# Kernel optimization log

Measured on AMD Instinct MI355X. Metric: run time of the kernel, lower is better.

The kernel has to match this reference:

```python
import jax, jax.numpy as jnp
import numpy as np
from jax import lax

B, S, D = 4, 2048, 512          # batch, doc seq len, input_size
Y = 8922                          # num labels (ICD codes)
V, E = 50000, 100                 # vocab, word embed dim
T, K = 32, 9                      # code-title tokens, conv filter size
PAD = K // 2


def setup_inputs() -> dict:
    key = jax.random.key(0)
    ks = jax.random.split(key, 8)
    x = jax.random.normal(ks[0], (B, S, D), dtype=jnp.float32)
    target = jax.random.randint(ks[1], (B, Y), 0, 2).astype(jnp.float32)
    c2title = jax.random.randint(ks[2], (Y, T), 0, V)
    embed_W = jax.random.normal(ks[3], (V, E), dtype=jnp.float32) * 0.1
    conv_w = jax.random.normal(ks[4], (D, E, K), dtype=jnp.float32) * 0.05  # [out, in, k]
    conv_b = jax.random.normal(ks[5], (D,), dtype=jnp.float32) * 0.05
    final_w = jax.random.normal(ks[6], (Y, D), dtype=jnp.float32) * 0.05
    final_b = jax.random.normal(ks[7], (Y,), dtype=jnp.float32) * 0.05
    return {"x": x, "target": target, "c2title": c2title, "embed_W": embed_W,
            "conv_w": conv_w, "conv_b": conv_b, "final_w": final_w, "final_b": final_b}


def reference(x, target, c2title, embed_W, conv_w, conv_b, final_w, final_b):
    # Code-title encoder: embed -> Conv1d (same padding) -> max-pool over time -> tanh
    ct = embed_W[c2title]                      # [Y, T, E]
    ct = jnp.transpose(ct, (0, 2, 1))          # [Y, E, T]  (NCH)
    U = lax.conv_general_dilated(ct, conv_w, window_strides=(1,),
                                 padding=[(PAD, PAD)],
                                 dimension_numbers=("NCH", "OIH", "NCH"))
    U = U + conv_b[None, :, None]              # [Y, D, T]
    U = jnp.tanh(jnp.max(U, axis=-1))          # [Y, D]  (MaxPool1d(T) + tanh)

    # Label cross-attention over document tokens
    scale = 1.0 / jnp.sqrt(jnp.float32(D))
    scores = jnp.einsum("yd,bsd->bys", U, x) * scale   # [B, Y, S]
    alpha = jax.nn.softmax(scores, axis=-1)             # softmax over seq
    m = jnp.einsum("bys,bsd->byd", alpha, x)            # [B, Y, D]

    # Per-label elementwise dot product + bias
    y = jnp.einsum("byd,yd->by", m, final_w) + final_b  # [B, Y]

    # BCEWithLogitsLoss (mean), numerically stable
    loss = jnp.mean(jnp.maximum(y, 0.0) - y * target + jnp.log1p(jnp.exp(-jnp.abs(y))))
    return (y, loss, alpha, m)
```

## Files before the change

### kernel.cpp

```cpp
#include <hip/hip_runtime.h>
#include <math.h>

#define BQ 4
#define SQ 2048
#define DQ 512
#define YQ 8922
#define TQ 32
#define EQ 100
#define EP 128
#define KQ 9
#define LD 128
#define YPAD 8960

typedef float f32x4 __attribute__((ext_vector_type(4)));
typedef short s16x8 __attribute__((ext_vector_type(8)));

static __device__ __forceinline__ f32x4 mfma16(s16x8 a, s16x8 b, f32x4 c) {
  return __builtin_amdgcn_mfma_f32_16x16x32_bf16(a, b, c, 0, 0, 0);
}

static __device__ __forceinline__ ushort f2bf(float f) {
  union { float f; unsigned u; } v; v.f = f;
  unsigned r = (v.u + 0x7FFFu + ((v.u >> 16) & 1u)) >> 16;
  return (ushort)r;
}

static __device__ __forceinline__ float bf2f(ushort h) {
  union { unsigned u; float f; } v; v.u = ((unsigned)h) << 16; return v.f;
}

static __device__ __forceinline__ f32x4 ld4u(const float* p) {
  f32x4 v; __builtin_memcpy(&v, p, 16); return v;
}
static __device__ __forceinline__ void st4u(float* p, f32x4 v) {
  __builtin_memcpy(p, &v, 16);
}

static __device__ __forceinline__ int swz_chunk(int row, int chunk) {
  return chunk ^ (row & 15);
}
static __device__ __forceinline__ int swz3(int row, int chunk) {
  return chunk ^ (row & 7);
}

__global__ void k_prep_x(const float* __restrict__ x, ushort* __restrict__ xb,
                         ushort* __restrict__ xT) {
  __shared__ ushort sm[64][66];
  int b = blockIdx.z;
  int s0 = blockIdx.x * 64;
  int d0 = blockIdx.y * 64;
  int tid = threadIdx.x;
  int sr = tid >> 4;
  int c4 = (tid & 15) * 4;
  #pragma unroll
  for (int it = 0; it < 4; ++it) {
    int s = sr + it * 16;
    f32x4 v = *(const f32x4*)(x + ((size_t)b * SQ + s0 + s) * DQ + d0 + c4);
    ushort4 h = make_ushort4(f2bf(v.x), f2bf(v.y), f2bf(v.z), f2bf(v.w));
    *(ushort4*)(xb + ((size_t)b * SQ + s0 + s) * DQ + d0 + c4) = h;
    sm[s][c4] = h.x; sm[s][c4 + 1] = h.y; sm[s][c4 + 2] = h.z; sm[s][c4 + 3] = h.w;
  }
  __syncthreads();
  #pragma unroll
  for (int it = 0; it < 4; ++it) {
    int d = sr + it * 16;
    ushort4 h;
    h.x = sm[c4][d]; h.y = sm[c4 + 1][d]; h.z = sm[c4 + 2][d]; h.w = sm[c4 + 3][d];
    *(ushort4*)(xT + ((size_t)b * DQ + d0 + d) * SQ + s0 + c4) = h;
  }
}

__global__ void k_pack_w(const float* __restrict__ cw, ushort* __restrict__ Wp) {
  int i = blockIdx.x * 256 + threadIdx.x;
  if (i >= KQ * DQ * EP) return;
  int e = i & (EP - 1);
  int d = (i >> 7) & (DQ - 1);
  int kk = i >> 16;
  float v = (e < EQ) ? cw[((size_t)d * EQ + e) * KQ + kk] : 0.f;
  Wp[i] = f2bf(v);
}

__launch_bounds__(256, 2)
__global__ void k_conv(const int* __restrict__ c2t, const float* __restrict__ embed,
                       const ushort* __restrict__ Wp, const float* __restrict__ cb,
                       ushort* __restrict__ U) {
  __shared__ ushort sA[4 * TQ * LD];
  __shared__ ushort sB[128 * LD];
  const f32x4 fz4 = {0.f, 0.f, 0.f, 0.f};
  const s16x8 sz8 = {0, 0, 0, 0, 0, 0, 0, 0};
  int tid = threadIdx.x;
  int d0 = blockIdx.x * 128;
  int y0 = blockIdx.y * 4;
  int lane = tid & 63, wave = tid >> 6;
  int wm = wave & 1, wn = wave >> 1;
  int lr = lane & 15, lg = lane >> 4;

  {
    int row = tid >> 1;
    int half = tid & 1;
    int yl = row >> 5, t = row & 31;
    int y = y0 + yl;
    const float* src = 0;
    if (y < YQ) src = embed + (size_t)c2t[y * TQ + t] * EQ + half * 64;
    #pragma unroll
    for (int j = 0; j < 16; ++j) {
      int col = half * 64 + j * 4;
      f32x4 v = fz4;
      if (src != 0 && col + 4 <= EQ) v = *(const f32x4*)(src + j * 4);
      ushort4 h = make_ushort4(f2bf(v.x), f2bf(v.y), f2bf(v.z), f2bf(v.w));
      int pc = swz_chunk(row, col >> 3);
      *(ushort4*)&sA[row * LD + pc * 8 + (col & 7)] = h;
    }
  }

  s16x8 breg[8];
  {
    const ushort* src = Wp + (size_t)d0 * EP;
    #pragma unroll
    for (int it = 0; it < 8; ++it) {
      int gi = tid + it * 256, r = gi >> 4, g = gi & 15;
      breg[it] = *(const s16x8*)(src + (size_t)r * EP + g * 8);
    }
    #pragma unroll
    for (int it = 0; it < 8; ++it) {
      int gi = tid + it * 256, r = gi >> 4, g = gi & 15;
      *(s16x8*)&sB[r * LD + swz_chunk(r, g) * 8] = breg[it];
    }
  }
  __syncthreads();

  f32x4 acc[4][4];
  #pragma unroll
  for (int i = 0; i < 4; ++i)
    #pragma unroll
    for (int j = 0; j < 4; ++j) acc[i][j] = fz4;

  for (int kk = 0; kk < KQ; ++kk) {
    if (kk + 1 < KQ) {
      const ushort* src = Wp + ((size_t)(kk + 1) * DQ + d0) * EP;
      #pragma unroll
      for (int it = 0; it < 8; ++it) {
        int gi = tid + it * 256, r = gi >> 4, g = gi & 15;
        breg[it] = *(const s16x8*)(src + (size_t)r * EP + g * 8);
      }
    }
    #pragma unroll
    for (int ee = 0; ee < 4; ++ee) {
      s16x8 af[4], bfr[4];
      #pragma unroll
      for (int i = 0; i < 4; ++i) {
        int rowm = wm * 64 + i * 16 + lr;
        int yl = rowm >> 5;
        int ts = (rowm & 31) + kk - 4;
        s16x8 a = sz8;
        if ((unsigned)ts < (unsigned)TQ) {
          int row = yl * TQ + ts;
          a = *(const s16x8*)&sA[row * LD + swz_chunk(row, ee * 4 + lg) * 8];
        }
        af[i] = a;
      }
      #pragma unroll
      for (int i = 0; i < 4; ++i) {
        int row = wn * 64 + i * 16 + lr;
        bfr[i] = *(const s16x8*)&sB[row * LD + swz_chunk(row, ee * 4 + lg) * 8];
      }
      #pragma unroll
      for (int i = 0; i < 4; ++i)
        #pragma unroll
        for (int j = 0; j < 4; ++j)
          acc[i][j] = mfma16(af[i], bfr[j], acc[i][j]);
    }
    __syncthreads();
    if (kk + 1 < KQ) {
      #pragma unroll
      for (int it = 0; it < 8; ++it) {
        int gi = tid + it * 256, r = gi >> 4, g = gi & 15;
        *(s16x8*)&sB[r * LD + swz_chunk(r, g) * 8] = breg[it];
      }
      __syncthreads();
    }
  }

  const float scl = 0.04419417382415922f;
  #pragma unroll
  for (int L2 = 0; L2 < 2; ++L2) {
    int y = y0 + wm * 2 + L2;
    #pragma unroll
    for (int j = 0; j < 4; ++j) {
      float mx = -3.0e38f;
      #pragma unroll
      for (int ii = 0; ii < 2; ++ii)
        #pragma unroll
        for (int q = 0; q < 4; ++q)
          mx = fmaxf(mx, acc[L2 * 2 + ii][j][q]);
      mx = fmaxf(mx, __shfl_xor(mx, 16));
      mx = fmaxf(mx, __shfl_xor(mx, 32));
      if (lane < 16 && y < YQ) {
        int col = d0 + wn * 64 + j * 16 + lane;
        U[(size_t)y * DQ + col] = f2bf(tanhf(mx + cb[col]) * scl);
      }
    }
  }
}

__launch_bounds__(256, 2)
__global__ void k_scores(const ushort* __restrict__ U, const ushort* __restrict__ xb,
                         float* __restrict__ sc, float* __restrict__ part) {
  __shared__ ushort sA[128 * LD];
  __shared__ ushort sB[128 * LD];
  const f32x4 fz4 = {0.f, 0.f, 0.f, 0.f};
  int tid = threadIdx.x;
  int s0 = blockIdx.x * 128;
  int y0 = blockIdx.y * 128;
  int b = blockIdx.z;
  const ushort* Ap = U + (size_t)y0 * DQ;
  const ushort* Bp = xb + ((size_t)b * SQ + s0) * DQ;
  f32x4 acc[4][4];
  #pragma unroll
  for (int i = 0; i < 4; ++i)
    #pragma unroll
    for (int j = 0; j < 4; ++j) acc[i][j] = fz4;
  int lane = tid & 63, wave = tid >> 6;
  int wm = wave & 1, wn = wave >> 1;
  int lr = lane & 15, lg = lane >> 4;

  for (int kc = 0; kc < DQ; kc += 128) {
    __syncthreads();
    #pragma unroll
    for (int it = 0; it < 8; ++it) {
      int gi = tid + it * 256;
      int r = gi >> 4, g = gi & 15;
      int pofs = r * LD + swz_chunk(r, g) * 8;
      *(s16x8*)&sA[pofs] = *(const s16x8*)(Ap + (size_t)r * DQ + kc + g * 8);
      *(s16x8*)&sB[pofs] = *(const s16x8*)(Bp + (size_t)r * DQ + kc + g * 8);
    }
    __syncthreads();
    #pragma unroll
    for (int ks = 0; ks < 4; ++ks) {
      s16x8 af[4], bfr[4];
      #pragma unroll
      for (int i = 0; i < 4; ++i) {
        int row = wm * 64 + i * 16 + lr;
        af[i] = *(const s16x8*)&sA[row * LD + swz_chunk(row, ks * 4 + lg) * 8];
      }
      #pragma unroll
      for (int i = 0; i < 4; ++i) {
        int row = wn * 64 + i * 16 + lr;
        bfr[i] = *(const s16x8*)&sB[row * LD + swz_chunk(row, ks * 4 + lg) * 8];
      }
      #pragma unroll
      for (int i = 0; i < 4; ++i)
        #pragma unroll
        for (int j = 0; j < 4; ++j)
          acc[i][j] = mfma16(af[i], bfr[j], acc[i][j]);
    }
  }
  float* out = sc + (size_t)b * YQ * SQ;
  int rb = wm * 64 + lg * 4;
  int cb_ = wn * 64 + lr;
  #pragma unroll
  for (int i = 0; i < 4; ++i)
    #pragma unroll
    for (int j = 0; j < 4; ++j) {
      int col = s0 + cb_ + j * 16;
      #pragma unroll
      for (int q = 0; q < 4; ++q) {
        int r = y0 + rb + i * 16 + q;
        if (r < YQ) out[(size_t)r * SQ + col] = acc[i][j][q];
      }
    }

  int hb = blockIdx.x * 2 + wn;
  #pragma unroll
  for (int i = 0; i < 4; ++i)
    #pragma unroll
    for (int q = 0; q < 4; ++q) {
      float mx = fmaxf(fmaxf(acc[i][0][q], acc[i][1][q]),
                       fmaxf(acc[i][2][q], acc[i][3][q]));
      #pragma unroll
      for (int o = 1; o < 16; o <<= 1) mx = fmaxf(mx, __shfl_xor(mx, o));
      float se = 0.f;
      #pragma unroll
      for (int j = 0; j < 4; ++j) se += __expf(acc[i][j][q] - mx);
      #pragma unroll
      for (int o = 1; o < 16; o <<= 1) se += __shfl_xor(se, o);
      int r = y0 + rb + i * 16 + q;
      if (lr == 0 && r < YQ) {
        float* pp = part + ((size_t)(b * YQ + r) * 32 + hb) * 2;
        pp[0] = mx;
        pp[1] = se;
      }
    }
}

__global__ void k_smfix(const float* __restrict__ part, float* __restrict__ rs) {
  int t = blockIdx.x * 256 + threadIdx.x;
  if (t >= BQ * YQ) return;
  const float* pp = part + (size_t)t * 64;
  float M = -3.0e38f;
  #pragma unroll
  for (int h = 0; h < 32; ++h) M = fmaxf(M, pp[h * 2]);
  float Z = 0.f;
  #pragma unroll
  for (int h = 0; h < 32; ++h) Z += __expf(pp[h * 2] - M) * pp[h * 2 + 1];
  rs[t * 2] = M;
  rs[t * 2 + 1] = 1.0f / Z;
}

__global__ void k_alpha(float* __restrict__ a, const float* __restrict__ rs,
                        ushort* __restrict__ abf) {
  int r = blockIdx.x;
  float M = rs[r * 2], iZ = rs[r * 2 + 1];
  float* p = a + (size_t)r * SQ;
  int tid = threadIdx.x;
  if (abf) {
    ushort* q = abf + (size_t)r * SQ;
    #pragma unroll
    for (int i = 0; i < 2; ++i) {
      int e = (tid + i * 256) * 4;
      f32x4 v = ld4u(p + e);
      ushort4 h;
      h.x = f2bf(__expf(v.x - M) * iZ);
      h.y = f2bf(__expf(v.y - M) * iZ);
      h.z = f2bf(__expf(v.z - M) * iZ);
      h.w = f2bf(__expf(v.w - M) * iZ);
      *(ushort4*)(q + e) = h;
    }
  } else {
    #pragma unroll
    for (int i = 0; i < 2; ++i) {
      int e = (tid + i * 256) * 4;
      f32x4 v = ld4u(p + e);
      v.x = __expf(v.x - M) * iZ;
      v.y = __expf(v.y - M) * iZ;
      v.z = __expf(v.z - M) * iZ;
      v.w = __expf(v.w - M) * iZ;
      st4u(p + e, v);
    }
  }
}

__launch_bounds__(512, 4)
__global__ void k_pv2(const ushort* __restrict__ abf, const ushort* __restrict__ xT,
                      float* __restrict__ mo, float* __restrict__ aout) {
  __shared__ ushort sA[128 * 64];
  __shared__ ushort sB[256 * 64];
  const f32x4 fz4 = {0.f, 0.f, 0.f, 0.f};
  const s16x8 sz8 = {0, 0, 0, 0, 0, 0, 0, 0};
  int tid = threadIdx.x;
  int d0 = blockIdx.x * 256;
  int y0 = blockIdx.y * 128;
  int b = blockIdx.z;
  int lane = tid & 63, wave = tid >> 6;
  int wm = wave >> 1;
  int wn = wave & 1;
  int lr = lane & 15, lg = lane >> 4;

  const ushort* Ap = abf + ((size_t)b * YQ + y0) * SQ;
  const ushort* Bp = xT + ((size_t)b * DQ + d0) * SQ;

  f32x4 acc[2][8];
  #pragma unroll
  for (int i = 0; i < 2; ++i)
    #pragma unroll
    for (int j = 0; j < 8; ++j) acc[i][j] = fz4;

  for (int kc = 0; kc < SQ; kc += 64) {
    bool wr_alpha = ((kc >> 10) == (int)blockIdx.x);
    #pragma unroll
    for (int p = 0; p < 2; ++p) {
      int u = tid + p * 512;
      int r = u >> 3, c = u & 7;
      int y = y0 + r;
      s16x8 v = sz8;
      if (y < YQ) {
        size_t base = (size_t)r * SQ + kc + c * 8;
        v = *(const s16x8*)(Ap + base);
        if (wr_alpha) {
          float* ao = aout + ((size_t)b * YQ + y) * SQ + kc + c * 8;
          f32x4 w0, w1;
          #pragma unroll
          for (int k2 = 0; k2 < 4; ++k2) w0[k2] = bf2f((ushort)v[k2]);
          #pragma unroll
          for (int k2 = 0; k2 < 4; ++k2) w1[k2] = bf2f((ushort)v[4 + k2]);
          st4u(ao, w0);
          st4u(ao + 4, w1);
        }
      }
      *(s16x8*)&sA[r * 64 + swz3(r, c) * 8] = v;
    }
    #pragma unroll
    for (int p = 0; p < 4; ++p) {
      int u = tid + p * 512;
      int r = u >> 3, c = u & 7;
      *(s16x8*)&sB[r * 64 + swz3(r, c) * 8] =
          *(const s16x8*)(Bp + (size_t)r * SQ + kc + c * 8);
    }
    __syncthreads();
    #pragma unroll
    for (int ks = 0; ks < 2; ++ks) {
      s16x8 af[2];
      #pragma unroll
      for (int i = 0; i < 2; ++i) {
        int row = wm * 32 + i * 16 + lr;
        af[i] = *(const s16x8*)&sA[row * 64 + swz3(row, ks * 4 + lg) * 8];
      }
      #pragma unroll
      for (int j = 0; j < 8; ++j) {
        int row = wn * 128 + j * 16 + lr;
        s16x8 bf = *(const s16x8*)&sB[row * 64 + swz3(row, ks * 4 + lg) * 8];
        acc[0][j] = mfma16(af[0], bf, acc[0][j]);
        acc[1][j] = mfma16(af[1], bf, acc[1][j]);
      }
    }
    __syncthreads();
  }

  float* out = mo + (size_t)b * YQ * DQ;
  #pragma unroll
  for (int i = 0; i < 2; ++i)
    #pragma unroll
    for (int q = 0; q < 4; ++q) {
      int r = y0 + wm * 32 + i * 16 + lg * 4 + q;
      if (r >= YQ) continue;
      #pragma unroll
      for (int j = 0; j < 8; ++j) {
        int col = d0 + wn * 128 + j * 16 + lr;
        out[(size_t)r * DQ + col] = acc[i][j][q];
      }
    }
}

__launch_bounds__(256, 2)
__global__ void k_pv(const float* __restrict__ alpha, const ushort* __restrict__ xT,
                     float* __restrict__ mo) {
  __shared__ ushort sA[128 * LD];
  __shared__ ushort sB[128 * LD];
  const f32x4 fz4 = {0.f, 0.f, 0.f, 0.f};
  int tid = threadIdx.x;
  int d0 = blockIdx.x * 128;
  int y0 = blockIdx.y * 128;
  int b = blockIdx.z;
  const float* Ap = alpha + ((size_t)b * YQ + y0) * SQ;
  const ushort* Bp = xT + ((size_t)b * DQ + d0) * SQ;
  f32x4 acc[4][4];
  #pragma unroll
  for (int i = 0; i < 4; ++i)
    #pragma unroll
    for (int j = 0; j < 4; ++j) acc[i][j] = fz4;
  int lane = tid & 63, wave = tid >> 6;
  int wm = wave & 1, wn = wave >> 1;
  int lr = lane & 15, lg = lane >> 4;

  for (int kc = 0; kc < SQ; kc += 128) {
    __syncthreads();
    #pragma unroll
    for (int it = 0; it < 8; ++it) {
      int gi = tid + it * 256;
      int r = gi >> 4, g = gi & 15;
      int y = y0 + r;
      int pofs = r * LD + swz_chunk(r, g) * 8;
      ushort4 h0 = make_ushort4(0, 0, 0, 0), h1 = make_ushort4(0, 0, 0, 0);
      if (y < YQ) {
        f32x4 v0 = ld4u(Ap + (size_t)r * SQ + kc + g * 8);
        f32x4 v1 = ld4u(Ap + (size_t)r * SQ + kc + g * 8 + 4);
        h0 = make_ushort4(f2bf(v0.x), f2bf(v0.y), f2bf(v0.z), f2bf(v0.w));
        h1 = make_ushort4(f2bf(v1.x), f2bf(v1.y), f2bf(v1.z), f2bf(v1.w));
      }
      *(ushort4*)&sA[pofs] = h0;
      *(ushort4*)&sA[pofs + 4] = h1;
      *(s16x8*)&sB[pofs] = *(const s16x8*)(Bp + (size_t)r * SQ + kc + g * 8);
    }
    __syncthreads();
    #pragma unroll
    for (int ks = 0; ks < 4; ++ks) {
      s16x8 af[4], bfr[4];
      #pragma unroll
      for (int i = 0; i < 4; ++i) {
        int row = wm * 64 + i * 16 + lr;
        af[i] = *(const s16x8*)&sA[row * LD + swz_chunk(row, ks * 4 + lg) * 8];
      }
      #pragma unroll
      for (int i = 0; i < 4; ++i) {
        int row = wn * 64 + i * 16 + lr;
        bfr[i] = *(const s16x8*)&sB[row * LD + swz_chunk(row, ks * 4 + lg) * 8];
      }
      #pragma unroll
      for (int i = 0; i < 4; ++i)
        #pragma unroll
        for (int j = 0; j < 4; ++j)
          acc[i][j] = mfma16(af[i], bfr[j], acc[i][j]);
    }
  }
  float* out = mo + (size_t)b * YQ * DQ;
  int rb = wm * 64 + lg * 4;
  int cb_ = wn * 64 + lr;
  #pragma unroll
  for (int i = 0; i < 4; ++i)
    #pragma unroll
    for (int j = 0; j < 4; ++j) {
      int col = d0 + cb_ + j * 16;
      #pragma unroll
      for (int q = 0; q < 4; ++q) {
        int r = y0 + rb + i * 16 + q;
        if (r < YQ) out[(size_t)r * DQ + col] = acc[i][j][q];
      }
    }
}

__global__ void k_final(const float* __restrict__ m_in, const float* __restrict__ fw,
                        const float* __restrict__ fb, const float* __restrict__ tgt,
                        float* __restrict__ yo, float* __restrict__ part) {
  int y = blockIdx.x;
  int lane = threadIdx.x & 63;
  int b = threadIdx.x >> 6;
  const float* mp = m_in + ((size_t)b * YQ + y) * DQ;
  const float* wp = fw + (size_t)y * DQ;
  float s = 0.f;
  #pragma unroll
  for (int i = 0; i < 8; ++i) {
    int e = lane + i * 64;
    s += mp[e] * wp[e];
  }
  #pragma unroll
  for (int o = 32; o > 0; o >>= 1) s += __shfl_xor(s, o);
  __shared__ float pl[4];
  if (lane == 0) {
    float yv = s + fb[y];
    yo[(size_t)b * YQ + y] = yv;
    float t = tgt[(size_t)b * YQ + y];
    pl[b] = fmaxf(yv, 0.f) - yv * t + log1pf(__expf(-fabsf(yv)));
  }
  __syncthreads();
  if (threadIdx.x == 0)
    part[y] = (pl[0] + pl[1]) + (pl[2] + pl[3]);
}

__global__ void k_loss_fin(const float* __restrict__ part, float* __restrict__ out) {
  int tid = threadIdx.x;
  float s = 0.f;
  for (int i = tid; i < YQ; i += 256) s += part[i];
  #pragma unroll
  for (int o = 32; o > 0; o >>= 1) s += __shfl_xor(s, o);
  __shared__ float red[4];
  int lane = tid & 63, wave = tid >> 6;
  if (lane == 0) red[wave] = s;
  __syncthreads();
  if (tid == 0)
    out[0] = ((red[0] + red[1]) + (red[2] + red[3])) * (1.0f / (float)(BQ * YQ));
}

extern "C" void kernel_launch(void* const* d_in, const int* in_sizes, int n_in,
                              void* d_out, int out_size, void* d_ws, size_t ws_size,
                              hipStream_t stream) {
  const float* x      = (const float*)d_in[0];
  const float* target = (const float*)d_in[1];
  const int*   c2t    = (const int*)d_in[2];
  const float* embed  = (const float*)d_in[3];
  const float* cw     = (const float*)d_in[4];
  const float* cb     = (const float*)d_in[5];
  const float* fw     = (const float*)d_in[6];
  const float* fb     = (const float*)d_in[7];

  char* ws = (char*)d_ws;
  ushort* xb   = (ushort*)(ws);
  ushort* xT   = (ushort*)(ws + 8388608);
  ushort* Wp   = (ushort*)(ws + 16777216);
  ushort* U    = (ushort*)(ws + 17956864);
  float* lpart = (float*)(ws + 27131904);
  float* part  = (float*)(ws + 27167744);
  float* rst   = (float*)(ws + 36303872);
  const size_t ABF_OFF = 36589568;
  const size_t NEED_ABF = ABF_OFF + (size_t)BQ * YQ * SQ * 2;
  bool use_abf = (ws_size >= NEED_ABF);
  ushort* abf = use_abf ? (ushort*)(ws + ABF_OFF) : (ushort*)0;

  float* out       = (float*)d_out;
  float* out_y     = out;
  float* out_loss  = out + (size_t)BQ * YQ;
  float* out_alpha = out + (size_t)BQ * YQ + 1;
  float* out_m     = out_alpha + (size_t)BQ * YQ * SQ;

  hipMemsetAsync(U, 0, (size_t)YPAD * DQ * 2, stream);

  k_prep_x<<<dim3(SQ / 64, DQ / 64, BQ), 256, 0, stream>>>(x, xb, xT);
  k_pack_w<<<dim3((KQ * DQ * EP + 255) / 256), 256, 0, stream>>>(cw, Wp);
  k_conv<<<dim3(4, (YQ + 3) / 4), 256, 0, stream>>>(c2t, embed, Wp, cb, U);
  k_scores<<<dim3(SQ / 128, (YQ + 127) / 128, BQ), 256, 0, stream>>>(U, xb, out_alpha, part);
  k_smfix<<<dim3((BQ * YQ + 255) / 256), 256, 0, stream>>>(part, rst);
  k_alpha<<<dim3(BQ * YQ), 256, 0, stream>>>(out_alpha, rst, abf);
  if (use_abf)
    k_pv2<<<dim3(DQ / 256, (YQ + 127) / 128, BQ), 512, 0, stream>>>(abf, xT, out_m, out_alpha);
  else
    k_pv<<<dim3(DQ / 128, (YQ + 127) / 128, BQ), 256, 0, stream>>>(out_alpha, xT, out_m);
  k_final<<<dim3(YQ), 256, 0, stream>>>(out_m, fw, fb, target, out_y, lpart);
  k_loss_fin<<<1, 256, 0, stream>>>(lpart, out_loss);
}
```

Measured before the change: 935.8 us.

## Fuse softmax normalization into scores and PV kernels with bf16 unnormalized probabilities

k_scores now writes bf16 exp(score minus local chunk max) instead of fp32 raw scores. k_smfix produces per-chunk rescale factors, and k_pv2 applies them while loading, emitting the fp32 alpha output itself. This removes the separate k_alpha pass and the fp32 score round trip through memory, roughly halving HBM traffic on the largest tensor. In exchange, alpha comes from values rounded to bf16 before rescaling, which may slightly reduce accuracy.

```diff
diff --git a/kernel.cpp b/kernel.cpp
--- a/kernel.cpp
+++ b/kernel.cpp
@@ -205,7 +205,8 @@
 
 __launch_bounds__(256, 2)
 __global__ void k_scores(const ushort* __restrict__ U, const ushort* __restrict__ xb,
-                         float* __restrict__ sc, float* __restrict__ part) {
+                         ushort* __restrict__ Pb, float* __restrict__ sc,
+                         float* __restrict__ part) {
   __shared__ ushort sA[128 * LD];
   __shared__ ushort sB[128 * LD];
   const f32x4 fz4 = {0.f, 0.f, 0.f, 0.f};
@@ -255,22 +256,11 @@
           acc[i][j] = mfma16(af[i], bfr[j], acc[i][j]);
     }
   }
-  float* out = sc + (size_t)b * YQ * SQ;
   int rb = wm * 64 + lg * 4;
   int cb_ = wn * 64 + lr;
-  #pragma unroll
-  for (int i = 0; i < 4; ++i)
-    #pragma unroll
-    for (int j = 0; j < 4; ++j) {
-      int col = s0 + cb_ + j * 16;
-      #pragma unroll
-      for (int q = 0; q < 4; ++q) {
-        int r = y0 + rb + i * 16 + q;
-        if (r < YQ) out[(size_t)r * SQ + col] = acc[i][j][q];
-      }
-    }
-
   int hb = blockIdx.x * 2 + wn;
+
+  float mxr[4][4];
   #pragma unroll
   for (int i = 0; i < 4; ++i)
     #pragma unroll
@@ -279,6 +269,7 @@
                        fmaxf(acc[i][2][q], acc[i][3][q]));
       #pragma unroll
       for (int o = 1; o < 16; o <<= 1) mx = fmaxf(mx, __shfl_xor(mx, o));
+      mxr[i][q] = mx;
       float se = 0.f;
       #pragma unroll
       for (int j = 0; j < 4; ++j) se += __expf(acc[i][j][q] - mx);
@@ -291,9 +282,39 @@
         pp[1] = se;
       }
     }
-}
-
-__global__ void k_smfix(const float* __restrict__ part, float* __restrict__ rs) {
+
+  if (Pb) {
+    ushort* out = Pb + (size_t)b * YQ * SQ;
+    #pragma unroll
+    for (int i = 0; i < 4; ++i)
+      #pragma unroll
+      for (int j = 0; j < 4; ++j) {
+        int col = s0 + cb_ + j * 16;
+        #pragma unroll
+        for (int q = 0; q < 4; ++q) {
+          int r = y0 + rb + i * 16 + q;
+          if (r < YQ)
+            out[(size_t)r * SQ + col] = f2bf(__expf(acc[i][j][q] - mxr[i][q]));
+        }
+      }
+  } else {
+    float* out = sc + (size_t)b * YQ * SQ;
+    #pragma unroll
+    for (int i = 0; i < 4; ++i)
+      #pragma unroll
+      for (int j = 0; j < 4; ++j) {
+        int col = s0 + cb_ + j * 16;
+        #pragma unroll
+        for (int q = 0; q < 4; ++q) {
+          int r = y0 + rb + i * 16 + q;
+          if (r < YQ) out[(size_t)r * SQ + col] = acc[i][j][q];
+        }
+      }
+  }
+}
+
+__global__ void k_smfix(const float* __restrict__ part, float* __restrict__ rs,
+                        float* __restrict__ rc) {
   int t = blockIdx.x * 256 + threadIdx.x;
   if (t >= BQ * YQ) return;
   const float* pp = part + (size_t)t * 64;
@@ -303,50 +324,40 @@
   float Z = 0.f;
   #pragma unroll
   for (int h = 0; h < 32; ++h) Z += __expf(pp[h * 2] - M) * pp[h * 2 + 1];
+  float iZ = 1.0f / Z;
   rs[t * 2] = M;
-  rs[t * 2 + 1] = 1.0f / Z;
-}
-
-__global__ void k_alpha(float* __restrict__ a, const float* __restrict__ rs,
-                        ushort* __restrict__ abf) {
+  rs[t * 2 + 1] = iZ;
+  if (rc) {
+    #pragma unroll
+    for (int h = 0; h < 32; ++h)
+      rc[(size_t)t * 32 + h] = __expf(pp[h * 2] - M) * iZ;
+  }
+}
+
+__global__ void k_alpha(float* __restrict__ a, const float* __restrict__ rs) {
   int r = blockIdx.x;
   float M = rs[r * 2], iZ = rs[r * 2 + 1];
   float* p = a + (size_t)r * SQ;
   int tid = threadIdx.x;
-  if (abf) {
-    ushort* q = abf + (size_t)r * SQ;
-    #pragma unroll
-    for (int i = 0; i < 2; ++i) {
-      int e = (tid + i * 256) * 4;
-      f32x4 v = ld4u(p + e);
-      ushort4 h;
-      h.x = f2bf(__expf(v.x - M) * iZ);
-      h.y = f2bf(__expf(v.y - M) * iZ);
-      h.z = f2bf(__expf(v.z - M) * iZ);
-      h.w = f2bf(__expf(v.w - M) * iZ);
-      *(ushort4*)(q + e) = h;
-    }
-  } else {
-    #pragma unroll
-    for (int i = 0; i < 2; ++i) {
-      int e = (tid + i * 256) * 4;
-      f32x4 v = ld4u(p + e);
-      v.x = __expf(v.x - M) * iZ;
-      v.y = __expf(v.y - M) * iZ;
-      v.z = __expf(v.z - M) * iZ;
-      v.w = __expf(v.w - M) * iZ;
-      st4u(p + e, v);
-    }
+  #pragma unroll
+  for (int i = 0; i < 2; ++i) {
+    int e = (tid + i * 256) * 4;
+    f32x4 v = ld4u(p + e);
+    v.x = __expf(v.x - M) * iZ;
+    v.y = __expf(v.y - M) * iZ;
+    v.z = __expf(v.z - M) * iZ;
+    v.w = __expf(v.w - M) * iZ;
+    st4u(p + e, v);
   }
 }
 
 __launch_bounds__(512, 4)
-__global__ void k_pv2(const ushort* __restrict__ abf, const ushort* __restrict__ xT,
-                      float* __restrict__ mo, float* __restrict__ aout) {
+__global__ void k_pv2(const ushort* __restrict__ Pb, const float* __restrict__ rc,
+                      const ushort* __restrict__ xT, float* __restrict__ mo,
+                      float* __restrict__ aout) {
   __shared__ ushort sA[128 * 64];
   __shared__ ushort sB[256 * 64];
   const f32x4 fz4 = {0.f, 0.f, 0.f, 0.f};
-  const s16x8 sz8 = {0, 0, 0, 0, 0, 0, 0, 0};
   int tid = threadIdx.x;
   int d0 = blockIdx.x * 256;
   int y0 = blockIdx.y * 128;
@@ -356,7 +367,7 @@
   int wn = wave & 1;
   int lr = lane & 15, lg = lane >> 4;
 
-  const ushort* Ap = abf + ((size_t)b * YQ + y0) * SQ;
+  const ushort* Ap = Pb + ((size_t)b * YQ + y0) * SQ;
   const ushort* Bp = xT + ((size_t)b * DQ + d0) * SQ;
 
   f32x4 acc[2][8];
@@ -367,27 +378,33 @@
 
   for (int kc = 0; kc < SQ; kc += 64) {
     bool wr_alpha = ((kc >> 10) == (int)blockIdx.x);
+    int hb = kc >> 6;
     #pragma unroll
     for (int p = 0; p < 2; ++p) {
       int u = tid + p * 512;
       int r = u >> 3, c = u & 7;
       int y = y0 + r;
-      s16x8 v = sz8;
+      ushort4 h0 = make_ushort4(0, 0, 0, 0), h1 = make_ushort4(0, 0, 0, 0);
       if (y < YQ) {
         size_t base = (size_t)r * SQ + kc + c * 8;
-        v = *(const s16x8*)(Ap + base);
+        s16x8 v = *(const s16x8*)(Ap + base);
+        float corr = rc[((size_t)(b * YQ + y)) * 32 + hb];
+        float pf[8];
+        #pragma unroll
+        for (int k2 = 0; k2 < 8; ++k2) pf[k2] = bf2f((ushort)v[k2]) * corr;
         if (wr_alpha) {
           float* ao = aout + ((size_t)b * YQ + y) * SQ + kc + c * 8;
-          f32x4 w0, w1;
-          #pragma unroll
-          for (int k2 = 0; k2 < 4; ++k2) w0[k2] = bf2f((ushort)v[k2]);
-          #pragma unroll
-          for (int k2 = 0; k2 < 4; ++k2) w1[k2] = bf2f((ushort)v[4 + k2]);
+          f32x4 w0 = {pf[0], pf[1], pf[2], pf[3]};
+          f32x4 w1 = {pf[4], pf[5], pf[6], pf[7]};
           st4u(ao, w0);
           st4u(ao + 4, w1);
         }
-      }
-      *(s16x8*)&sA[r * 64 + swz3(r, c) * 8] = v;
+        h0 = make_ushort4(f2bf(pf[0]), f2bf(pf[1]), f2bf(pf[2]), f2bf(pf[3]));
+        h1 = make_ushort4(f2bf(pf[4]), f2bf(pf[5]), f2bf(pf[6]), f2bf(pf[7]));
+      }
+      int pofs = r * 64 + swz3(r, c) * 8;
+      *(ushort4*)&sA[pofs] = h0;
+      *(ushort4*)&sA[pofs + 4] = h1;
     }
     #pragma unroll
     for (int p = 0; p < 4; ++p) {
@@ -570,10 +587,11 @@
   float* lpart = (float*)(ws + 27131904);
   float* part  = (float*)(ws + 27167744);
   float* rst   = (float*)(ws + 36303872);
-  const size_t ABF_OFF = 36589568;
-  const size_t NEED_ABF = ABF_OFF + (size_t)BQ * YQ * SQ * 2;
-  bool use_abf = (ws_size >= NEED_ABF);
-  ushort* abf = use_abf ? (ushort*)(ws + ABF_OFF) : (ushort*)0;
+  float* rc    = (float*)(ws + 36589568);
+  const size_t PB_OFF = 41157632;
+  const size_t NEED_F = PB_OFF + (size_t)BQ * YQ * SQ * 2;
+  bool fused = (ws_size >= NEED_F);
+  ushort* Pb = fused ? (ushort*)(ws + PB_OFF) : (ushort*)0;
 
   float* out       = (float*)d_out;
   float* out_y     = out;
@@ -586,13 +604,18 @@
   k_prep_x<<<dim3(SQ / 64, DQ / 64, BQ), 256, 0, stream>>>(x, xb, xT);
   k_pack_w<<<dim3((KQ * DQ * EP + 255) / 256), 256, 0, stream>>>(cw, Wp);
   k_conv<<<dim3(4, (YQ + 3) / 4), 256, 0, stream>>>(c2t, embed, Wp, cb, U);
-  k_scores<<<dim3(SQ / 128, (YQ + 127) / 128, BQ), 256, 0, stream>>>(U, xb, out_alpha, part);
-  k_smfix<<<dim3((BQ * YQ + 255) / 256), 256, 0, stream>>>(part, rst);
-  k_alpha<<<dim3(BQ * YQ), 256, 0, stream>>>(out_alpha, rst, abf);
-  if (use_abf)
-    k_pv2<<<dim3(DQ / 256, (YQ + 127) / 128, BQ), 512, 0, stream>>>(abf, xT, out_m, out_alpha);
-  else
-    k_pv<<<dim3(DQ / 128, (YQ + 127) / 128, BQ), 256, 0, stream>>>(out_alpha, xT, out_m);
+  k_scores<<<dim3(SQ / 128, (YQ + 127) / 128, BQ), 256, 0, stream>>>(
+      U, xb, Pb, out_alpha, part);
+  k_smfix<<<dim3((BQ * YQ + 255) / 256), 256, 0, stream>>>(part, rst,
+                                                           fused ? rc : (float*)0);
+  if (fused) {
+    k_pv2<<<dim3(DQ / 256, (YQ + 127) / 128, BQ), 512, 0, stream>>>(
+        Pb, rc, xT, out_m, out_alpha);
+  } else {
+    k_alpha<<<dim3(BQ * YQ), 256, 0, stream>>>(out_alpha, rst);
+    k_pv<<<dim3(DQ / 128, (YQ + 127) / 128, BQ), 256, 0, stream>>>(
+        out_alpha, xT, out_m);
+  }
   k_final<<<dim3(YQ), 256, 0, stream>>>(out_m, fw, fb, target, out_y, lpart);
   k_loss_fin<<<1, 256, 0, stream>>>(lpart, out_loss);
 }
```

Measured after the change: 855.0 us. 8.6% less time.
